# Kernel optimization log

Hardware: AMD Instinct MI355X
Metric: run time of the kernel (lower is better)

Reference implementation:

```python
import jax, jax.numpy as jnp
import numpy as np

ALPHA = 0.5   # leak rate
GAMMA = 0.01  # input scaling
RHO = 1.0     # target spectral radius
SPARSITY = 0.9  # fraction of zeros in W

T, N_INPUT, N_OUTPUT = 4096, 8192, 2048


def setup_inputs() -> dict:
    key = jax.random.key(0)
    k1, k2, k3, k4 = jax.random.split(key, 4)
    x = jax.random.normal(k1, (T, N_INPUT), dtype=jnp.float32)
    Win = GAMMA * jax.random.normal(k2, (N_INPUT, N_OUTPUT), dtype=jnp.float32)
    mask = (jax.random.uniform(k3, (N_OUTPUT, N_OUTPUT)) < (1.0 - SPARSITY)).astype(jnp.float32)
    W0 = jax.random.normal(k4, (N_OUTPUT, N_OUTPUT), dtype=jnp.float32) * mask
    # spectral-radius normalization (circular-law estimate: radius ~ sqrt(p * N) for
    # density p), standing in for rho * W / max|eig(W)| at init time.
    W = RHO * W0 / jnp.sqrt((1.0 - SPARSITY) * N_OUTPUT)
    return {"x": x, "W": W, "Win": Win}


def reference(x, W, Win):
    # x: [T, nInput]; output: [T, nOutput] (stacked hidden states)
    u_proj = x @ Win  # [T, nOutput], input projection is independent of the recurrence

    def step(v, up):
        # v: [nOutput]  leaky-integrator reservoir update
        v_new = (1.0 - ALPHA) * v + ALPHA * jnp.tanh(v @ W + up)
        return v_new, v_new

    v0 = jnp.zeros((W.shape[0],), dtype=x.dtype)  # ESN starts from zero state
    _, vs = jax.lax.scan(step, v0, u_proj)
    return vs
```

## Files before the change

### kernel.cpp

```cpp
#include <hip/hip_runtime.h>
#include <hip/hip_bf16.h>
#include <math.h>

#define T_STEPS 4096
#define N_IN    8192
#define N_OUT   2048

#define GM_BK 16

__global__ __launch_bounds__(256) void gemm_xwin(const float* __restrict__ X,
                                                 const float* __restrict__ Win,
                                                 float* __restrict__ U) {
    const int K = N_IN, N = N_OUT;
    __shared__ float As[GM_BK][128 + 4];
    __shared__ float Bs[GM_BK][128 + 4];

    const int tid = threadIdx.x;
    const int bm = blockIdx.x;
    const int bn = blockIdx.y;
    const int tx = tid & 15;
    const int ty = tid >> 4;

    float acc[8][8];
#pragma unroll
    for (int i = 0; i < 8; i++)
#pragma unroll
        for (int j = 0; j < 8; j++) acc[i][j] = 0.f;

    const float* Xb = X + (size_t)(bm * 128) * K;
    const float* Wb = Win + bn * 128;

    for (int kt = 0; kt < K; kt += GM_BK) {
#pragma unroll
        for (int q = 0; q < 2; q++) {
            const int r  = (tid >> 2) + q * 64;
            const int c4 = (tid & 3) * 4;
            const float4 a4 = *reinterpret_cast<const float4*>(&Xb[(size_t)r * K + kt + c4]);
            As[c4 + 0][r] = a4.x;
            As[c4 + 1][r] = a4.y;
            As[c4 + 2][r] = a4.z;
            As[c4 + 3][r] = a4.w;
        }
#pragma unroll
        for (int q = 0; q < 2; q++) {
            const int r  = (tid >> 5) + q * 8;
            const int c4 = (tid & 31) * 4;
            *reinterpret_cast<float4*>(&Bs[r][c4]) =
                *reinterpret_cast<const float4*>(&Wb[(size_t)(kt + r) * N + c4]);
        }
        __syncthreads();

#pragma unroll
        for (int k = 0; k < GM_BK; k++) {
            float a[8], b[8];
#pragma unroll
            for (int i = 0; i < 4; i++) {
                a[i]     = As[k][ty * 4 + i];
                a[4 + i] = As[k][64 + ty * 4 + i];
            }
#pragma unroll
            for (int j = 0; j < 4; j++) {
                b[j]     = Bs[k][tx * 4 + j];
                b[4 + j] = Bs[k][64 + tx * 4 + j];
            }
#pragma unroll
            for (int i = 0; i < 8; i++)
#pragma unroll
                for (int j = 0; j < 8; j++)
                    acc[i][j] = fmaf(a[i], b[j], acc[i][j]);
        }
        __syncthreads();
    }

#pragma unroll
    for (int i = 0; i < 8; i++) {
        const int mr = bm * 128 + ((i < 4) ? (ty * 4 + i) : (64 + ty * 4 + (i - 4)));
        float* Crow = U + (size_t)mr * N + bn * 128;
        float4 v0 = make_float4(acc[i][0], acc[i][1], acc[i][2], acc[i][3]);
        float4 v1 = make_float4(acc[i][4], acc[i][5], acc[i][6], acc[i][7]);
        *reinterpret_cast<float4*>(&Crow[tx * 4])      = v0;
        *reinterpret_cast<float4*>(&Crow[64 + tx * 4]) = v1;
    }
}

#define RB   64
#define CPB  32
#define GRP  8
#define CAP  288
#define KMAX (CAP / GRP)

__device__ __forceinline__ float fast_tanh(float x) {
    const float ax = fabsf(x);
    const float e  = __expf(2.0f * ax);
    const float r  = __builtin_amdgcn_rcpf(e + 1.0f);
    const float t  = 1.0f - 2.0f * r;
    return copysignf(t, x);
}

__global__ __launch_bounds__(256, 1) void esn_recur(const float* __restrict__ W,
                                                    float* __restrict__ UO,
                                                    unsigned long long* vslots) {
    __shared__ unsigned long long ent[CPB][CAP];
    __shared__ int   cnts[CPB];
    __shared__ float vsh[2][N_OUT];

    const int tid = threadIdx.x;
    const int b   = blockIdx.x;
    const int c   = tid >> 3;
    const int l   = tid & 7;
    const int j   = b * CPB + c;

    int cnt = 0;
    for (int k = 0; k < N_OUT / GRP; k++) {
        const float w = W[(size_t)(l + GRP * k) * N_OUT + j];
        cnt += (w != 0.0f) ? 1 : 0;
    }
    int inc = cnt;
#pragma unroll
    for (int d = 1; d < GRP; d <<= 1) {
        int n = __shfl_up(inc, d, 64);
        if (l >= d) inc += n;
    }
    int pos = inc - cnt;
    if (l == GRP - 1) cnts[c] = inc;
    for (int k = 0; k < N_OUT / GRP; k++) {
        const int i = l + GRP * k;
        const float w = W[(size_t)i * N_OUT + j];
        if (w != 0.0f) {
            if (pos < CAP)
                ent[c][pos] = ((unsigned long long)(unsigned)i << 32) | __float_as_uint(w);
            pos++;
        }
    }
    __syncthreads();
    const int ccnt = min(cnts[c], CAP);

    float wreg[KMAX];
    int   ireg[KMAX];
#pragma unroll
    for (int k = 0; k < KMAX; k++) {
        const int p = l + k * GRP;
        if (p < ccnt) {
            const unsigned long long e = ent[c][p];
            wreg[k] = __uint_as_float((unsigned)e);
            ireg[k] = (int)(e >> 32);
        } else {
            wreg[k] = 0.f;
            ireg[k] = 0;
        }
    }

#pragma unroll 1
    for (int t = 0; t < T_STEPS; t++) {
        float u = 0.f;
        if (l == 0) u = UO[(size_t)t * N_OUT + j];

        unsigned long long* vin = vslots + (size_t)(t & 1) * N_OUT;
        float* dst = vsh[t & 1];
        unsigned long long uq[8];
#pragma unroll
        for (int q = 0; q < 8; q++)
            uq[q] = __hip_atomic_load(&vin[tid + q * 256], __ATOMIC_RELAXED,
                                      __HIP_MEMORY_SCOPE_AGENT);
        unsigned pend = 0xFFu;
#pragma unroll 1
        while (true) {
            unsigned np = 0;
#pragma unroll
            for (int q = 0; q < 8; q++) {
                if (pend & (1u << q)) {
                    if ((unsigned)(uq[q] >> 32) == (unsigned)t)
                        dst[tid + q * 256] = __uint_as_float((unsigned)uq[q]);
                    else
                        np |= (1u << q);
                }
            }
            pend = np;
            if (!pend) break;
#pragma unroll
            for (int q = 0; q < 8; q++)
                if (pend & (1u << q))
                    uq[q] = __hip_atomic_load(&vin[tid + q * 256], __ATOMIC_RELAXED,
                                              __HIP_MEMORY_SCOPE_AGENT);
        }
        __syncthreads();

        const float* vcur = vsh[t & 1];
        float y0 = 0.f, y1 = 0.f, y2 = 0.f, y3 = 0.f;
#pragma unroll
        for (int k = 0; k < KMAX; k += 4) {
            y0 = fmaf(wreg[k + 0], vcur[ireg[k + 0]], y0);
            y1 = fmaf(wreg[k + 1], vcur[ireg[k + 1]], y1);
            y2 = fmaf(wreg[k + 2], vcur[ireg[k + 2]], y2);
            y3 = fmaf(wreg[k + 3], vcur[ireg[k + 3]], y3);
        }
        float y = (y0 + y1) + (y2 + y3);
#pragma unroll
        for (int d = GRP / 2; d >= 1; d >>= 1) y += __shfl_xor(y, d, 64);

        if (l == 0) {
            const float vnew = 0.5f * vcur[j] + 0.5f * fast_tanh(y + u);
            const unsigned long long slot =
                ((unsigned long long)(unsigned)(t + 1) << 32) | __float_as_uint(vnew);
            __hip_atomic_store(&vslots[(size_t)((t + 1) & 1) * N_OUT + j], slot,
                               __ATOMIC_RELAXED, __HIP_MEMORY_SCOPE_AGENT);
            UO[(size_t)t * N_OUT + j] = vnew;
        }
    }
}

extern "C" void kernel_launch(void* const* d_in, const int* in_sizes, int n_in,
                              void* d_out, int out_size, void* d_ws, size_t ws_size,
                              hipStream_t stream) {
    const float* x   = (const float*)d_in[0];
    const float* W   = (const float*)d_in[1];
    const float* Win = (const float*)d_in[2];
    float* out = (float*)d_out;

    unsigned long long* vslots = (unsigned long long*)d_ws;

    hipMemsetAsync(d_ws, 0, 2 * N_OUT * sizeof(unsigned long long), stream);

    dim3 ggrid(T_STEPS / 128, N_OUT / 128);
    gemm_xwin<<<ggrid, 256, 0, stream>>>(x, Win, out);

    esn_recur<<<RB, 256, 0, stream>>>(W, out, vslots);
}
```

Baseline: 13.37 ms.

## Gather needed reservoir values directly from global slots, removing block barrier

The recurrence kernel no longer copies the full 2048-entry state into shared memory behind a __syncthreads. Each lane now polls only the global slots for the nonzero column indices it needs, plus its own previous value, and leaves the wait loop once the whole wavefront is satisfied. The change also doubles the block count while halving columns per block (16 lanes per column), and grows the slot ring from 2 to 4 buffers. The aim is to cut per-step barrier and full-state copy latency on the serial critical path. The cost is scattered global atomic loads, about 18 per lane per step, instead of coalesced ones, and 128 persistent blocks that must all be co-resident.

```diff
diff --git a/kernel.cpp b/kernel.cpp
--- a/kernel.cpp
+++ b/kernel.cpp
@@ -83,9 +83,9 @@
     }
 }
 
-#define RB   64
-#define CPB  32
-#define GRP  8
+#define RB   128
+#define CPB  16
+#define GRP  16
 #define CAP  288
 #define KMAX (CAP / GRP)
 
@@ -101,13 +101,12 @@
                                                     float* __restrict__ UO,
                                                     unsigned long long* vslots) {
     __shared__ unsigned long long ent[CPB][CAP];
-    __shared__ int   cnts[CPB];
-    __shared__ float vsh[2][N_OUT];
+    __shared__ int cnts[CPB];
 
     const int tid = threadIdx.x;
     const int b   = blockIdx.x;
-    const int c   = tid >> 3;
-    const int l   = tid & 7;
+    const int c   = tid >> 4;
+    const int l   = tid & 15;
     const int j   = b * CPB + c;
 
     int cnt = 0;
@@ -136,73 +135,89 @@
     const int ccnt = min(cnts[c], CAP);
 
     float wreg[KMAX];
-    int   ireg[KMAX];
+    int   idx[KMAX];
+    unsigned valid = 0;
 #pragma unroll
     for (int k = 0; k < KMAX; k++) {
         const int p = l + k * GRP;
         if (p < ccnt) {
             const unsigned long long e = ent[c][p];
             wreg[k] = __uint_as_float((unsigned)e);
-            ireg[k] = (int)(e >> 32);
+            idx[k]  = (int)(e >> 32);
+            valid |= (1u << k);
         } else {
             wreg[k] = 0.f;
-            ireg[k] = 0;
+            idx[k]  = 0;
         }
     }
 
 #pragma unroll 1
     for (int t = 0; t < T_STEPS; t++) {
+        const unsigned long long* vin = vslots + (size_t)(t & 3) * N_OUT;
+
         float u = 0.f;
         if (l == 0) u = UO[(size_t)t * N_OUT + j];
 
-        unsigned long long* vin = vslots + (size_t)(t & 1) * N_OUT;
-        float* dst = vsh[t & 1];
-        unsigned long long uq[8];
-#pragma unroll
-        for (int q = 0; q < 8; q++)
-            uq[q] = __hip_atomic_load(&vin[tid + q * 256], __ATOMIC_RELAXED,
-                                      __HIP_MEMORY_SCOPE_AGENT);
-        unsigned pend = 0xFFu;
+        unsigned long long uq[KMAX];
+        float val[KMAX];
+        unsigned pend = valid;
+        bool pend_s = (l == 0);
+        unsigned long long uqs = 0;
+        float vold = 0.f;
+#pragma unroll
+        for (int k = 0; k < KMAX; k++) val[k] = 0.f;
+
+#pragma unroll
+        for (int k = 0; k < KMAX; k++)
+            if (pend & (1u << k))
+                uq[k] = __hip_atomic_load(&vin[idx[k]], __ATOMIC_RELAXED,
+                                          __HIP_MEMORY_SCOPE_AGENT);
+        if (pend_s)
+            uqs = __hip_atomic_load(&vin[j], __ATOMIC_RELAXED,
+                                    __HIP_MEMORY_SCOPE_AGENT);
+
 #pragma unroll 1
         while (true) {
-            unsigned np = 0;
-#pragma unroll
-            for (int q = 0; q < 8; q++) {
-                if (pend & (1u << q)) {
-                    if ((unsigned)(uq[q] >> 32) == (unsigned)t)
-                        dst[tid + q * 256] = __uint_as_float((unsigned)uq[q]);
-                    else
-                        np |= (1u << q);
+#pragma unroll
+            for (int k = 0; k < KMAX; k++) {
+                if (pend & (1u << k)) {
+                    if ((unsigned)(uq[k] >> 32) == (unsigned)t) {
+                        val[k] = __uint_as_float((unsigned)uq[k]);
+                        pend &= ~(1u << k);
+                    }
                 }
             }
-            pend = np;
-            if (!pend) break;
-#pragma unroll
-            for (int q = 0; q < 8; q++)
-                if (pend & (1u << q))
-                    uq[q] = __hip_atomic_load(&vin[tid + q * 256], __ATOMIC_RELAXED,
+            if (pend_s && (unsigned)(uqs >> 32) == (unsigned)t) {
+                vold = __uint_as_float((unsigned)uqs);
+                pend_s = false;
+            }
+            if (!__any(pend != 0 || pend_s)) break;
+#pragma unroll
+            for (int k = 0; k < KMAX; k++)
+                if (pend & (1u << k))
+                    uq[k] = __hip_atomic_load(&vin[idx[k]], __ATOMIC_RELAXED,
                                               __HIP_MEMORY_SCOPE_AGENT);
-        }
-        __syncthreads();
-
-        const float* vcur = vsh[t & 1];
-        float y0 = 0.f, y1 = 0.f, y2 = 0.f, y3 = 0.f;
-#pragma unroll
-        for (int k = 0; k < KMAX; k += 4) {
-            y0 = fmaf(wreg[k + 0], vcur[ireg[k + 0]], y0);
-            y1 = fmaf(wreg[k + 1], vcur[ireg[k + 1]], y1);
-            y2 = fmaf(wreg[k + 2], vcur[ireg[k + 2]], y2);
-            y3 = fmaf(wreg[k + 3], vcur[ireg[k + 3]], y3);
-        }
-        float y = (y0 + y1) + (y2 + y3);
+            if (pend_s)
+                uqs = __hip_atomic_load(&vin[j], __ATOMIC_RELAXED,
+                                        __HIP_MEMORY_SCOPE_AGENT);
+        }
+
+        float y0 = 0.f, y1 = 0.f, y2 = 0.f;
+#pragma unroll
+        for (int k = 0; k < KMAX; k += 3) {
+            y0 = fmaf(wreg[k + 0], val[k + 0], y0);
+            y1 = fmaf(wreg[k + 1], val[k + 1], y1);
+            y2 = fmaf(wreg[k + 2], val[k + 2], y2);
+        }
+        float y = (y0 + y1) + y2;
 #pragma unroll
         for (int d = GRP / 2; d >= 1; d >>= 1) y += __shfl_xor(y, d, 64);
 
         if (l == 0) {
-            const float vnew = 0.5f * vcur[j] + 0.5f * fast_tanh(y + u);
+            const float vnew = 0.5f * vold + 0.5f * fast_tanh(y + u);
             const unsigned long long slot =
                 ((unsigned long long)(unsigned)(t + 1) << 32) | __float_as_uint(vnew);
-            __hip_atomic_store(&vslots[(size_t)((t + 1) & 1) * N_OUT + j], slot,
+            __hip_atomic_store(&vslots[(size_t)((t + 1) & 3) * N_OUT + j], slot,
                                __ATOMIC_RELAXED, __HIP_MEMORY_SCOPE_AGENT);
             UO[(size_t)t * N_OUT + j] = vnew;
         }
@@ -219,7 +234,7 @@
 
     unsigned long long* vslots = (unsigned long long*)d_ws;
 
-    hipMemsetAsync(d_ws, 0, 2 * N_OUT * sizeof(unsigned long long), stream);
+    hipMemsetAsync(d_ws, 0, 4 * N_OUT * sizeof(unsigned long long), stream);
 
     dim3 ggrid(T_STEPS / 128, N_OUT / 128);
     gemm_xwin<<<ggrid, 256, 0, stream>>>(x, Win, out);
```

Result: slower. 27.00 ms (+102.0%).

## Run recurrence as 256 single-wave blocks with a 4-slot state ring

Applied to the files above, without the earlier changes.

Splits the recurrent kernel into 256 one-wavefront blocks of 8 columns each instead of 64 four-wave blocks. This removes the per-step __syncthreads, keeps each block's previous state in a register, and gathers column sums with a cross-lane shuffle. The double-buffered state slots become a 4-slot ring. The intent is to cut per-step barrier latency in the serial 4096-step chain. In exchange, each lane now polls 32 global slots per step, and four times as many blocks poll, which raises L2 traffic.

```diff
diff --git a/kernel.cpp b/kernel.cpp
--- a/kernel.cpp
+++ b/kernel.cpp
@@ -83,11 +83,12 @@
     }
 }
 
-#define RB   64
-#define CPB  32
+#define RB   256
+#define CPB  8
 #define GRP  8
 #define CAP  288
 #define KMAX (CAP / GRP)
+#define QSL  (N_OUT / 64)
 
 __device__ __forceinline__ float fast_tanh(float x) {
     const float ax = fabsf(x);
@@ -97,12 +98,12 @@
     return copysignf(t, x);
 }
 
-__global__ __launch_bounds__(256, 1) void esn_recur(const float* __restrict__ W,
-                                                    float* __restrict__ UO,
-                                                    unsigned long long* vslots) {
+__global__ __launch_bounds__(64, 1) void esn_recur(const float* __restrict__ W,
+                                                   float* __restrict__ UO,
+                                                   unsigned long long* vslots) {
     __shared__ unsigned long long ent[CPB][CAP];
     __shared__ int   cnts[CPB];
-    __shared__ float vsh[2][N_OUT];
+    __shared__ float vsh[N_OUT];
 
     const int tid = threadIdx.x;
     const int b   = blockIdx.x;
@@ -150,61 +151,67 @@
         }
     }
 
+    float vold = 0.f;
+
 #pragma unroll 1
     for (int t = 0; t < T_STEPS; t++) {
         float u = 0.f;
-        if (l == 0) u = UO[(size_t)t * N_OUT + j];
-
-        unsigned long long* vin = vslots + (size_t)(t & 1) * N_OUT;
-        float* dst = vsh[t & 1];
-        unsigned long long uq[8];
-#pragma unroll
-        for (int q = 0; q < 8; q++)
-            uq[q] = __hip_atomic_load(&vin[tid + q * 256], __ATOMIC_RELAXED,
+        if (l == 0) u = UO[(size_t)t * N_OUT + j] * 0.f + u;
+        u = 0.f;
+        if (tid < CPB) u = UO[(size_t)t * N_OUT + b * CPB + tid];
+
+        const unsigned long long* vin = vslots + (size_t)(t & 3) * N_OUT;
+        unsigned long long uq[QSL];
+#pragma unroll
+        for (int q = 0; q < QSL; q++)
+            uq[q] = __hip_atomic_load(&vin[tid + q * 64], __ATOMIC_RELAXED,
                                       __HIP_MEMORY_SCOPE_AGENT);
-        unsigned pend = 0xFFu;
+        unsigned pend = 0xFFFFFFFFu;
 #pragma unroll 1
         while (true) {
             unsigned np = 0;
 #pragma unroll
-            for (int q = 0; q < 8; q++) {
+            for (int q = 0; q < QSL; q++) {
                 if (pend & (1u << q)) {
                     if ((unsigned)(uq[q] >> 32) == (unsigned)t)
-                        dst[tid + q * 256] = __uint_as_float((unsigned)uq[q]);
+                        vsh[tid + q * 64] = __uint_as_float((unsigned)uq[q]);
                     else
                         np |= (1u << q);
                 }
             }
             pend = np;
-            if (!pend) break;
-#pragma unroll
-            for (int q = 0; q < 8; q++)
+            if (!__any(pend != 0)) break;
+#pragma unroll
+            for (int q = 0; q < QSL; q++)
                 if (pend & (1u << q))
-                    uq[q] = __hip_atomic_load(&vin[tid + q * 256], __ATOMIC_RELAXED,
+                    uq[q] = __hip_atomic_load(&vin[tid + q * 64], __ATOMIC_RELAXED,
                                               __HIP_MEMORY_SCOPE_AGENT);
         }
-        __syncthreads();
-
-        const float* vcur = vsh[t & 1];
+
         float y0 = 0.f, y1 = 0.f, y2 = 0.f, y3 = 0.f;
 #pragma unroll
         for (int k = 0; k < KMAX; k += 4) {
-            y0 = fmaf(wreg[k + 0], vcur[ireg[k + 0]], y0);
-            y1 = fmaf(wreg[k + 1], vcur[ireg[k + 1]], y1);
-            y2 = fmaf(wreg[k + 2], vcur[ireg[k + 2]], y2);
-            y3 = fmaf(wreg[k + 3], vcur[ireg[k + 3]], y3);
+            y0 = fmaf(wreg[k + 0], vsh[ireg[k + 0]], y0);
+            y1 = fmaf(wreg[k + 1], vsh[ireg[k + 1]], y1);
+            y2 = fmaf(wreg[k + 2], vsh[ireg[k + 2]], y2);
+            y3 = fmaf(wreg[k + 3], vsh[ireg[k + 3]], y3);
         }
         float y = (y0 + y1) + (y2 + y3);
 #pragma unroll
         for (int d = GRP / 2; d >= 1; d >>= 1) y += __shfl_xor(y, d, 64);
 
-        if (l == 0) {
-            const float vnew = 0.5f * vcur[j] + 0.5f * fast_tanh(y + u);
+        const float ycol = __shfl(y, (tid * 8) & 63, 64);
+
+        if (tid < CPB) {
+            const int jj = b * CPB + tid;
+            const float vnew = 0.5f * vold + 0.5f * fast_tanh(ycol + u);
+            vold = vnew;
             const unsigned long long slot =
                 ((unsigned long long)(unsigned)(t + 1) << 32) | __float_as_uint(vnew);
-            __hip_atomic_store(&vslots[(size_t)((t + 1) & 1) * N_OUT + j], slot,
+            __hip_atomic_store(&vslots[(size_t)((t + 1) & 3) * N_OUT + jj], slot,
                                __ATOMIC_RELAXED, __HIP_MEMORY_SCOPE_AGENT);
-            UO[(size_t)t * N_OUT + j] = vnew;
+            __hip_atomic_store(&UO[(size_t)t * N_OUT + jj], vnew,
+                               __ATOMIC_RELAXED, __HIP_MEMORY_SCOPE_AGENT);
         }
     }
 }
@@ -219,10 +226,10 @@
 
     unsigned long long* vslots = (unsigned long long*)d_ws;
 
-    hipMemsetAsync(d_ws, 0, 2 * N_OUT * sizeof(unsigned long long), stream);
+    hipMemsetAsync(d_ws, 0, 4 * N_OUT * sizeof(unsigned long long), stream);
 
     dim3 ggrid(T_STEPS / 128, N_OUT / 128);
     gemm_xwin<<<ggrid, 256, 0, stream>>>(x, Win, out);
 
-    esn_recur<<<RB, 256, 0, stream>>>(W, out, vslots);
-}
+    esn_recur<<<RB, 64, 0, stream>>>(W, out, vslots);
+}
```

New measurement: 31.54 ms. +136.0%, slower.

## Confine recurrence to one XCD with ticketed blocks and L2-local polling

Applied to the files above, without the earlier changes.

The recurrent kernel now launches many blocks, exits every block that is not on XCC 0, and assigns 32 partitions through an atomic ticket, so all cross-block exchange of the hidden state stays within one XCD's L2. Polling uses inline-asm sc0 loads over 8 contiguous slots per thread, with a fallback to a device-scope mirror buffer after several rounds. It also keeps the previous state in a register, prefetches the next input projection, and uses 4-slot rotation with 4 lanes per output column. The intent is to cut per-step inter-block synchronisation latency. The risks are relying on XCC placement, non-coherent polling that could stall or hang, and fewer active CUs.

```diff
diff --git a/kernel.cpp b/kernel.cpp
--- a/kernel.cpp
+++ b/kernel.cpp
@@ -83,11 +83,12 @@
     }
 }
 
-#define RB   64
-#define CPB  32
-#define GRP  8
-#define CAP  288
-#define KMAX (CAP / GRP)
+#define NPART 32
+#define CPB   64
+#define GRP   4
+#define CAP   288
+#define KMAX  (CAP / GRP)
+#define SCN   16
 
 __device__ __forceinline__ float fast_tanh(float x) {
     const float ax = fabsf(x);
@@ -97,93 +98,145 @@
     return copysignf(t, x);
 }
 
+__device__ __forceinline__ unsigned xcc_id() {
+    unsigned x;
+    asm("s_getreg_b32 %0, hwreg(HW_REG_XCC_ID)" : "=s"(x));
+    return x;
+}
+
+#define POLL8(pp)                                                        \
+    asm volatile(                                                        \
+        "global_load_dwordx2 %0, %8, off sc0\n\t"                        \
+        "global_load_dwordx2 %1, %8, off offset:8 sc0\n\t"               \
+        "global_load_dwordx2 %2, %8, off offset:16 sc0\n\t"              \
+        "global_load_dwordx2 %3, %8, off offset:24 sc0\n\t"              \
+        "global_load_dwordx2 %4, %8, off offset:32 sc0\n\t"              \
+        "global_load_dwordx2 %5, %8, off offset:40 sc0\n\t"              \
+        "global_load_dwordx2 %6, %8, off offset:48 sc0\n\t"              \
+        "global_load_dwordx2 %7, %8, off offset:56 sc0\n\t"              \
+        "s_waitcnt vmcnt(0)"                                             \
+        : "=&v"(q0), "=&v"(q1), "=&v"(q2), "=&v"(q3),                    \
+          "=&v"(q4), "=&v"(q5), "=&v"(q6), "=&v"(q7)                     \
+        : "v"(pp)                                                        \
+        : "memory")
+
+#define CHK(i, qi)                                                       \
+    if (pend & (1u << i)) {                                              \
+        if ((unsigned)((qi) >> 32) == ut)                                \
+            dst[base + i] = __uint_as_float((unsigned)(qi));             \
+        else                                                             \
+            np |= (1u << i);                                             \
+    }
+
+#define MIRR(i, qi)                                                      \
+    if (pend & (1u << i))                                                \
+        qi = __hip_atomic_load(&vmir[base + i], __ATOMIC_RELAXED,        \
+                               __HIP_MEMORY_SCOPE_AGENT);
+
 __global__ __launch_bounds__(256, 1) void esn_recur(const float* __restrict__ W,
                                                     float* __restrict__ UO,
-                                                    unsigned long long* vslots) {
-    __shared__ unsigned long long ent[CPB][CAP];
-    __shared__ int   cnts[CPB];
+                                                    unsigned long long* vprim,
+                                                    unsigned long long* vmirror,
+                                                    int* ticket) {
+    __shared__ unsigned long long ent[SCN][CAP];
+    __shared__ int   cnts[SCN];
     __shared__ float vsh[2][N_OUT];
+    __shared__ int   tk_sh;
+
+    if (xcc_id() != 0) return;
+    if (threadIdx.x == 0) tk_sh = atomicAdd(ticket, 1);
+    __syncthreads();
+    const int b = tk_sh;
+    if (b >= NPART) return;
 
     const int tid = threadIdx.x;
-    const int b   = blockIdx.x;
-    const int c   = tid >> 3;
-    const int l   = tid & 7;
+    const int c   = tid >> 2;
+    const int l   = tid & 3;
     const int j   = b * CPB + c;
-
-    int cnt = 0;
-    for (int k = 0; k < N_OUT / GRP; k++) {
-        const float w = W[(size_t)(l + GRP * k) * N_OUT + j];
-        cnt += (w != 0.0f) ? 1 : 0;
-    }
-    int inc = cnt;
-#pragma unroll
-    for (int d = 1; d < GRP; d <<= 1) {
-        int n = __shfl_up(inc, d, 64);
-        if (l >= d) inc += n;
-    }
-    int pos = inc - cnt;
-    if (l == GRP - 1) cnts[c] = inc;
-    for (int k = 0; k < N_OUT / GRP; k++) {
-        const int i = l + GRP * k;
-        const float w = W[(size_t)i * N_OUT + j];
-        if (w != 0.0f) {
-            if (pos < CAP)
-                ent[c][pos] = ((unsigned long long)(unsigned)i << 32) | __float_as_uint(w);
-            pos++;
-        }
-    }
-    __syncthreads();
-    const int ccnt = min(cnts[c], CAP);
+    const int wave = tid >> 6;
 
     float wreg[KMAX];
     int   ireg[KMAX];
-#pragma unroll
-    for (int k = 0; k < KMAX; k++) {
-        const int p = l + k * GRP;
-        if (p < ccnt) {
-            const unsigned long long e = ent[c][p];
-            wreg[k] = __uint_as_float((unsigned)e);
-            ireg[k] = (int)(e >> 32);
-        } else {
-            wreg[k] = 0.f;
-            ireg[k] = 0;
-        }
-    }
-
 #pragma unroll 1
-    for (int t = 0; t < T_STEPS; t++) {
-        float u = 0.f;
-        if (l == 0) u = UO[(size_t)t * N_OUT + j];
-
-        unsigned long long* vin = vslots + (size_t)(t & 1) * N_OUT;
+    for (int chunk = 0; chunk < 4; ++chunk) {
+        const int jc = b * CPB + chunk * SCN + (tid >> 4);
+        const int sl = tid & 15;
+        int cnt = 0;
+        for (int k = 0; k < N_OUT / 16; ++k)
+            cnt += (W[(size_t)(sl + 16 * k) * N_OUT + jc] != 0.f) ? 1 : 0;
+        int inc = cnt;
+#pragma unroll
+        for (int d = 1; d < 16; d <<= 1) {
+            int n = __shfl_up(inc, d, 64);
+            if (sl >= d) inc += n;
+        }
+        int pos = inc - cnt;
+        if (sl == 15) cnts[tid >> 4] = inc;
+        for (int k = 0; k < N_OUT / 16; ++k) {
+            const int i = sl + 16 * k;
+            const float w = W[(size_t)i * N_OUT + jc];
+            if (w != 0.f) {
+                if (pos < CAP)
+                    ent[tid >> 4][pos] =
+                        ((unsigned long long)(unsigned)i << 32) | __float_as_uint(w);
+                pos++;
+            }
+        }
+        __syncthreads();
+        if (wave == chunk) {
+            const int cc   = c & 15;
+            const int ccnt = min(cnts[cc], CAP);
+#pragma unroll
+            for (int k = 0; k < KMAX; ++k) {
+                const int p = l + k * GRP;
+                if (p < ccnt) {
+                    const unsigned long long e = ent[cc][p];
+                    wreg[k] = __uint_as_float((unsigned)e);
+                    ireg[k] = (int)(e >> 32);
+                } else {
+                    wreg[k] = 0.f;
+                    ireg[k] = 0;
+                }
+            }
+        }
+        __syncthreads();
+    }
+
+    float vold  = 0.f;
+    float u_cur = 0.f;
+    if (l == 0) u_cur = UO[j];
+
+#pragma unroll 1
+    for (int t = 0; t < T_STEPS; ++t) {
+        unsigned long long* vin = vprim + (size_t)(t & 3) * N_OUT;
+        const unsigned long long* vmir = vmirror + (size_t)(t & 3) * N_OUT;
         float* dst = vsh[t & 1];
-        unsigned long long uq[8];
-#pragma unroll
-        for (int q = 0; q < 8; q++)
-            uq[q] = __hip_atomic_load(&vin[tid + q * 256], __ATOMIC_RELAXED,
-                                      __HIP_MEMORY_SCOPE_AGENT);
+        const int base = tid * 8;
+        const unsigned ut = (unsigned)t;
+
+        unsigned long long q0, q1, q2, q3, q4, q5, q6, q7;
+        const unsigned long long* pp = vin + base;
+        POLL8(pp);
         unsigned pend = 0xFFu;
+        int rounds = 0;
 #pragma unroll 1
         while (true) {
             unsigned np = 0;
-#pragma unroll
-            for (int q = 0; q < 8; q++) {
-                if (pend & (1u << q)) {
-                    if ((unsigned)(uq[q] >> 32) == (unsigned)t)
-                        dst[tid + q * 256] = __uint_as_float((unsigned)uq[q]);
-                    else
-                        np |= (1u << q);
-                }
-            }
+            CHK(0, q0) CHK(1, q1) CHK(2, q2) CHK(3, q3)
+            CHK(4, q4) CHK(5, q5) CHK(6, q6) CHK(7, q7)
             pend = np;
             if (!pend) break;
-#pragma unroll
-            for (int q = 0; q < 8; q++)
-                if (pend & (1u << q))
-                    uq[q] = __hip_atomic_load(&vin[tid + q * 256], __ATOMIC_RELAXED,
-                                              __HIP_MEMORY_SCOPE_AGENT);
-        }
-        __syncthreads();
+            if (++rounds < 6) {
+                POLL8(pp);
+            } else {
+                MIRR(0, q0) MIRR(1, q1) MIRR(2, q2) MIRR(3, q3)
+                MIRR(4, q4) MIRR(5, q5) MIRR(6, q6) MIRR(7, q7)
+            }
+        }
+        __syncthreads();
+
+        float u_nxt = 0.f;
+        if (l == 0 && t + 1 < T_STEPS) u_nxt = UO[(size_t)(t + 1) * N_OUT + j];
 
         const float* vcur = vsh[t & 1];
         float y0 = 0.f, y1 = 0.f, y2 = 0.f, y3 = 0.f;
@@ -195,17 +248,22 @@
             y3 = fmaf(wreg[k + 3], vcur[ireg[k + 3]], y3);
         }
         float y = (y0 + y1) + (y2 + y3);
-#pragma unroll
-        for (int d = GRP / 2; d >= 1; d >>= 1) y += __shfl_xor(y, d, 64);
+        y += __shfl_xor(y, 2, 64);
+        y += __shfl_xor(y, 1, 64);
 
         if (l == 0) {
-            const float vnew = 0.5f * vcur[j] + 0.5f * fast_tanh(y + u);
+            const float vnew = 0.5f * vold + 0.5f * fast_tanh(y + u_cur);
+            vold = vnew;
             const unsigned long long slot =
                 ((unsigned long long)(unsigned)(t + 1) << 32) | __float_as_uint(vnew);
-            __hip_atomic_store(&vslots[(size_t)((t + 1) & 1) * N_OUT + j], slot,
+            unsigned long long* pd = vprim + (size_t)((t + 1) & 3) * N_OUT + j;
+            asm volatile("global_store_dwordx2 %0, %1, off sc0"
+                         :: "v"(pd), "v"(slot) : "memory");
+            __hip_atomic_store(&vmirror[(size_t)((t + 1) & 3) * N_OUT + j], slot,
                                __ATOMIC_RELAXED, __HIP_MEMORY_SCOPE_AGENT);
             UO[(size_t)t * N_OUT + j] = vnew;
         }
+        u_cur = u_nxt;
     }
 }
 
@@ -217,12 +275,14 @@
     const float* Win = (const float*)d_in[2];
     float* out = (float*)d_out;
 
-    unsigned long long* vslots = (unsigned long long*)d_ws;
-
-    hipMemsetAsync(d_ws, 0, 2 * N_OUT * sizeof(unsigned long long), stream);
+    unsigned long long* vprim   = (unsigned long long*)d_ws;
+    unsigned long long* vmirror = vprim + 4 * N_OUT;
+    int* ticket = (int*)((char*)d_ws + 8 * N_OUT * sizeof(unsigned long long));
+
+    hipMemsetAsync(d_ws, 0, 8 * N_OUT * sizeof(unsigned long long) + 64, stream);
 
     dim3 ggrid(T_STEPS / 128, N_OUT / 128);
     gemm_xwin<<<ggrid, 256, 0, stream>>>(x, Win, out);
 
-    esn_recur<<<RB, 256, 0, stream>>>(W, out, vslots);
-}
+    esn_recur<<<1024, 256, 0, stream>>>(W, out, vprim, vmirror, ticket);
+}
```

New measurement: 36.39 ms. 2.72x slower.
